# Optimization experiments

Measured on AMD Instinct MI355X. Metric: run time of the kernel, lower is better.

The kernel has to match this reference:

```python
import jax, jax.numpy as jnp
import numpy as np

B, N, H = 2, 2048, 1024
NUM_HEADS = 16
HEAD_DIM = H // NUM_HEADS
SCALE = HEAD_DIM ** -0.5


def setup_inputs() -> dict:
    key = jax.random.key(0)
    k1, k2, k3, k4 = jax.random.split(key, 4)
    s = 0.02
    return {
        "x": jax.random.normal(k1, (B, N, H), dtype=jnp.float32),
        "x2": jax.random.normal(k2, (B, N, H), dtype=jnp.float32),
        "Wqkv": jax.random.normal(k3, (H, 3 * H), dtype=jnp.float32) * s,
        "Wout": jax.random.normal(k4, (H, H), dtype=jnp.float32) * s,
        "bout": jnp.zeros((H,), dtype=jnp.float32),
    }


def _split_qkv(t):
    # t: [B, N, 3H] -> [3, B, h, N, d]
    b, n, _ = t.shape
    t = t.reshape(b, n, 3, NUM_HEADS, HEAD_DIM)
    return jnp.transpose(t, (2, 0, 3, 1, 4))


def reference(x, x2, Wqkv, Wout, bout):
    # shared qkv projection applied to both streams (bias=False)
    qkv2 = _split_qkv(x2 @ Wqkv)  # k, v from x2
    k, v = qkv2[1], qkv2[2]       # [B, h, N2, d]
    qkv1 = _split_qkv(x @ Wqkv)   # q from x
    q = qkv1[0]                   # [B, h, N, d]

    att = jax.nn.softmax(jnp.einsum("bhxd,bhyd->bhxy", q, k) * SCALE, axis=-1)
    out = jnp.einsum("bhxy,bhyd->bhxd", att, v)        # [B, h, N, d]
    out = jnp.transpose(out, (0, 2, 1, 3)).reshape(x.shape[0], x.shape[1], -1)
    return out @ Wout + bout
```

## Files before the change

### kernel.cpp

```cpp
#include <hip/hip_runtime.h>

#define B_ 2
#define N_ 2048
#define H_ 1024
#define NH_ 16
#define D_ 64

typedef _Float16 f16;
typedef _Float16 f16x4 __attribute__((ext_vector_type(4)));
typedef _Float16 f16x8 __attribute__((ext_vector_type(8)));
typedef float f32x4 __attribute__((ext_vector_type(4)));

#define MFMA16(a, b, c) __builtin_amdgcn_mfma_f32_16x16x32_f16((a), (b), (c), 0, 0, 0)

__device__ __forceinline__ void cp16(void* lds, const void* g) {
  __builtin_amdgcn_global_load_lds(
      (const __attribute__((address_space(1))) void*)g,
      (__attribute__((address_space(3))) void*)lds, 16, 0, 0);
}

__global__ __launch_bounds__(256) void convf16(
    const float* __restrict__ a, const float* __restrict__ b,
    f16* __restrict__ ao, f16* __restrict__ bo) {
  const size_t i = ((size_t)blockIdx.x * 256 + threadIdx.x) * 8;
  const float* __restrict__ src = (blockIdx.y == 0) ? a : b;
  f16* __restrict__ dst = (blockIdx.y == 0) ? ao : bo;
  float4 v0 = ((const float4*)(src + i))[0];
  float4 v1 = ((const float4*)(src + i))[1];
  f16x8 o;
  o[0] = (f16)v0.x; o[1] = (f16)v0.y; o[2] = (f16)v0.z; o[3] = (f16)v0.w;
  o[4] = (f16)v1.x; o[5] = (f16)v1.y; o[6] = (f16)v1.z; o[7] = (f16)v1.w;
  *(f16x8*)(dst + i) = o;
}

__global__ __launch_bounds__(256) void transw(
    const float* __restrict__ W, f16* __restrict__ Wt, int rows, int ncols) {
  const int cb = blockIdx.x * 64, kb = blockIdx.y * 64;
  const int t = threadIdx.x;
  __shared__ f16 T[64][72];
  {
    const int k = t >> 2, c0 = (t & 3) * 16;
    const float* wp = W + (size_t)(kb + k) * ncols + cb + c0;
    float4 w0 = ((const float4*)wp)[0];
    float4 w1 = ((const float4*)wp)[1];
    float4 w2 = ((const float4*)wp)[2];
    float4 w3 = ((const float4*)wp)[3];
    T[c0 + 0][k] = (f16)w0.x;  T[c0 + 1][k] = (f16)w0.y;
    T[c0 + 2][k] = (f16)w0.z;  T[c0 + 3][k] = (f16)w0.w;
    T[c0 + 4][k] = (f16)w1.x;  T[c0 + 5][k] = (f16)w1.y;
    T[c0 + 6][k] = (f16)w1.z;  T[c0 + 7][k] = (f16)w1.w;
    T[c0 + 8][k] = (f16)w2.x;  T[c0 + 9][k] = (f16)w2.y;
    T[c0 + 10][k] = (f16)w2.z; T[c0 + 11][k] = (f16)w2.w;
    T[c0 + 12][k] = (f16)w3.x; T[c0 + 13][k] = (f16)w3.y;
    T[c0 + 14][k] = (f16)w3.z; T[c0 + 15][k] = (f16)w3.w;
  }
  __syncthreads();
  {
    const int c = t >> 2, k0 = (t & 3) * 16;
    f16* op = Wt + (size_t)(cb + c) * rows + kb + k0;
    *(f16x8*)(op + 0) = *(const f16x8*)(&T[c][k0]);
    *(f16x8*)(op + 8) = *(const f16x8*)(&T[c][k0 + 8]);
  }
}

__global__ __launch_bounds__(256) void transv(
    const f16* __restrict__ V, f16* __restrict__ Vt) {
  const int nb = blockIdx.x * 64, bh = blockIdx.y;
  const int t = threadIdx.x;
  __shared__ f16 T[64][72];
  {
    const int n = t >> 2, d0 = (t & 3) * 16;
    const f16* vp = V + ((size_t)bh * N_ + nb + n) * D_ + d0;
    f16x8 v0 = *(const f16x8*)(vp);
    f16x8 v1 = *(const f16x8*)(vp + 8);
#pragma unroll
    for (int i = 0; i < 8; ++i) T[d0 + i][n] = v0[i];
#pragma unroll
    for (int i = 0; i < 8; ++i) T[d0 + 8 + i][n] = v1[i];
  }
  __syncthreads();
  {
    const int d = t >> 2, n0 = (t & 3) * 16;
    f16* op = Vt + ((size_t)bh * D_ + d) * N_ + nb + n0;
    *(f16x8*)(op + 0) = *(const f16x8*)(&T[d][n0]);
    *(f16x8*)(op + 8) = *(const f16x8*)(&T[d][n0 + 8]);
  }
}

__global__ __launch_bounds__(256) void qkv_mfma(
    const f16* __restrict__ Xc, const f16* __restrict__ X2c,
    const f16* __restrict__ Wt, f16* __restrict__ Qo,
    f16* __restrict__ Ko, f16* __restrict__ Vo) {
  const int bid = blockIdx.x;
  const int rb = (bid & 31) * 128;
  const int cb = (bid >> 5) * 128;
  const int t = threadIdx.x;
  const int lane = t & 63, wid = t >> 6;
  const int quad = lane >> 4, n16 = lane & 15;
  const int wm = wid >> 1, wn = wid & 1;

  const f16* __restrict__ A = (cb < H_) ? Xc : X2c;
  const int seg = cb >> 10;
  const float qscale = (seg == 0) ? 0.125f * 1.44269504f : 1.0f;
  f16* __restrict__ outp = (seg == 0) ? Qo : (seg == 1 ? Ko : Vo);

  __shared__ f16 As[128 * 32];
  __shared__ f16 Bs[128 * 32];

  f32x4 acc[4][4];
#pragma unroll
  for (int i = 0; i < 4; ++i)
#pragma unroll
    for (int j = 0; j < 4; ++j) acc[i][j] = (f32x4){0.f, 0.f, 0.f, 0.f};

  int srow0 = wid * 16 + (lane >> 2);
  int srow1 = 64 + srow0;
  int gl0 = ((lane & 3) ^ ((srow0 >> 1) & 3)) * 8;
  int gl1 = ((lane & 3) ^ ((srow1 >> 1) & 3)) * 8;
  const f16* gA0 = A + (size_t)(rb + srow0) * H_ + gl0;
  const f16* gA1 = A + (size_t)(rb + srow1) * H_ + gl1;
  const f16* gB0 = Wt + (size_t)(cb + srow0) * H_ + gl0;
  const f16* gB1 = Wt + (size_t)(cb + srow1) * H_ + gl1;
  f16* lA0 = &As[wid * 512];
  f16* lA1 = &As[2048 + wid * 512];
  f16* lB0 = &Bs[wid * 512];
  f16* lB1 = &Bs[2048 + wid * 512];

  const int fsw = (quad ^ ((n16 >> 1) & 3)) * 8;
  int aoff[4], boff[4];
#pragma unroll
  for (int i = 0; i < 4; ++i) {
    aoff[i] = (wm * 64 + i * 16 + n16) * 32 + fsw;
    boff[i] = (wn * 64 + i * 16 + n16) * 32 + fsw;
  }

  for (int kt = 0; kt < H_; kt += 32) {
    __syncthreads();
    cp16(lA0, gA0); cp16(lA1, gA1);
    cp16(lB0, gB0); cp16(lB1, gB1);
    gA0 += 32; gA1 += 32; gB0 += 32; gB1 += 32;
    __syncthreads();

    f16x8 af[4], bf[4];
#pragma unroll
    for (int mt = 0; mt < 4; ++mt) af[mt] = *(const f16x8*)(&As[aoff[mt]]);
#pragma unroll
    for (int nt = 0; nt < 4; ++nt) bf[nt] = *(const f16x8*)(&Bs[boff[nt]]);
#pragma unroll
    for (int mt = 0; mt < 4; ++mt)
#pragma unroll
      for (int nt = 0; nt < 4; ++nt)
        acc[mt][nt] = MFMA16(af[mt], bf[nt], acc[mt][nt]);
  }

#pragma unroll
  for (int mt = 0; mt < 4; ++mt)
#pragma unroll
    for (int nt = 0; nt < 4; ++nt)
#pragma unroll
      for (int r = 0; r < 4; ++r) {
        int grow = rb + wm * 64 + mt * 16 + quad * 4 + r;
        int gcol = cb + wn * 64 + nt * 16 + n16;
        int bb = grow >> 11, nn = grow & 2047;
        int hh = (gcol >> 6) & 15, dd = gcol & 63;
        outp[(((size_t)(bb * NH_ + hh)) * N_ + nn) * D_ + dd] =
            (f16)(acc[mt][nt][r] * qscale);
      }
}

__global__ __launch_bounds__(256) void attn2(
    const f16* __restrict__ Q, const f16* __restrict__ K,
    const f16* __restrict__ Vt, f16* __restrict__ AO) {
  const int bh = blockIdx.y;
  const int b = bh >> 4, h = bh & 15;
  const int qb = blockIdx.x * 128;
  const int t = threadIdx.x;
  const int lane = t & 63, wid = t >> 6;
  const int quad = lane >> 4, n16 = lane & 15;

  const f16* __restrict__ Qp = Q + (size_t)bh * N_ * D_;
  const f16* __restrict__ Kp = K + (size_t)bh * N_ * D_;
  const f16* __restrict__ Vp = Vt + (size_t)bh * D_ * N_;

  __shared__ f16 Ks[64 * 64];
  __shared__ f16 Vs[64 * 64];
  __shared__ f16 Ps[4][32 * 72];

  f16x8 qf[2][2];
#pragma unroll
  for (int qc = 0; qc < 2; ++qc) {
    const f16* qp = Qp + (size_t)(qb + wid * 32 + qc * 16 + n16) * D_ + quad * 8;
    qf[qc][0] = *(const f16x8*)(qp);
    qf[qc][1] = *(const f16x8*)(qp + 32);
  }

  f32x4 o[2][4];
#pragma unroll
  for (int i = 0; i < 2; ++i)
#pragma unroll
    for (int j = 0; j < 4; ++j) o[i][j] = (f32x4){0.f, 0.f, 0.f, 0.f};
  float lsum[2] = {0.f, 0.f};

  int srow0 = wid * 8 + (lane >> 3);
  int srow1 = 32 + srow0;
  int gl0 = ((lane & 7) ^ (srow0 & 7)) * 8;
  int gl1 = ((lane & 7) ^ (srow1 & 7)) * 8;
  const f16* gK0 = Kp + (size_t)srow0 * D_ + gl0;
  const f16* gK1 = Kp + (size_t)srow1 * D_ + gl1;
  const f16* gV0 = Vp + (size_t)srow0 * N_ + gl0;
  const f16* gV1 = Vp + (size_t)srow1 * N_ + gl1;
  f16* lK0 = &Ks[wid * 512];
  f16* lK1 = &Ks[2048 + wid * 512];
  f16* lV0 = &Vs[wid * 512];
  f16* lV1 = &Vs[2048 + wid * 512];

  const int fs0 = (quad ^ (n16 & 7)) * 8;
  const int fs1 = ((quad + 4) ^ (n16 & 7)) * 8;

  for (int kt = 0; kt < N_; kt += 64) {
    __syncthreads();
    cp16(lK0, gK0); cp16(lK1, gK1);
    cp16(lV0, gV0); cp16(lV1, gV1);
    gK0 += 64 * D_; gK1 += 64 * D_; gV0 += 64; gV1 += 64;
    __syncthreads();

    f32x4 s[4][2];
#pragma unroll
    for (int kc = 0; kc < 4; ++kc) {
      const f16x8 kf0 = *(const f16x8*)(&Ks[(kc * 16 + n16) * 64 + fs0]);
      const f16x8 kf1 = *(const f16x8*)(&Ks[(kc * 16 + n16) * 64 + fs1]);
#pragma unroll
      for (int qc = 0; qc < 2; ++qc) {
        f32x4 sv = (f32x4){0.f, 0.f, 0.f, 0.f};
        sv = MFMA16(kf0, qf[qc][0], sv);
        sv = MFMA16(kf1, qf[qc][1], sv);
        s[kc][qc] = sv;
      }
    }

    f16* __restrict__ pw = Ps[wid];
#pragma unroll
    for (int qc = 0; qc < 2; ++qc) {
      float ls = 0.f;
#pragma unroll
      for (int kc = 0; kc < 4; ++kc) {
        f16x4 pk;
#pragma unroll
        for (int r = 0; r < 4; ++r) {
          float p = __builtin_amdgcn_exp2f(s[kc][qc][r]);
          ls += p;
          pk[r] = (f16)p;
        }
        *(f16x4*)(&pw[(qc * 16 + n16) * 72 + kc * 16 + quad * 4]) = pk;
      }
      lsum[qc] += ls;
    }

    f16x8 vf[4][2];
#pragma unroll
    for (int dt = 0; dt < 4; ++dt) {
      vf[dt][0] = *(const f16x8*)(&Vs[(dt * 16 + n16) * 64 + fs0]);
      vf[dt][1] = *(const f16x8*)(&Vs[(dt * 16 + n16) * 64 + fs1]);
    }
#pragma unroll
    for (int mq = 0; mq < 2; ++mq) {
      const f16x8 pa0 = *(const f16x8*)(&pw[(mq * 16 + n16) * 72 + quad * 8]);
      const f16x8 pa1 = *(const f16x8*)(&pw[(mq * 16 + n16) * 72 + 32 + quad * 8]);
#pragma unroll
      for (int dt = 0; dt < 4; ++dt) {
        o[mq][dt] = MFMA16(pa0, vf[dt][0], o[mq][dt]);
        o[mq][dt] = MFMA16(pa1, vf[dt][1], o[mq][dt]);
      }
    }
  }

#pragma unroll
  for (int qc = 0; qc < 2; ++qc) {
    lsum[qc] += __shfl_xor(lsum[qc], 16);
    lsum[qc] += __shfl_xor(lsum[qc], 32);
  }

#pragma unroll
  for (int mq = 0; mq < 2; ++mq)
#pragma unroll
    for (int r = 0; r < 4; ++r) {
      float inv = 1.0f / __shfl(lsum[mq], quad * 4 + r);
      int nrow = qb + wid * 32 + mq * 16 + quad * 4 + r;
      f16* aop = AO + ((size_t)(b * N_ + nrow)) * H_ + h * 64;
#pragma unroll
      for (int dt = 0; dt < 4; ++dt)
        aop[dt * 16 + n16] = (f16)(o[mq][dt][r] * inv);
    }
}

__global__ __launch_bounds__(256) void out_mfma(
    const f16* __restrict__ A, const f16* __restrict__ Wt,
    const float* __restrict__ bias, float* __restrict__ out) {
  const int bid = blockIdx.x;
  const int rb = (bid & 31) * 128;
  const int cb = (bid >> 5) * 128;
  const int t = threadIdx.x;
  const int lane = t & 63, wid = t >> 6;
  const int quad = lane >> 4, n16 = lane & 15;
  const int wm = wid >> 1, wn = wid & 1;

  __shared__ f16 As[128 * 32];
  __shared__ f16 Bs[128 * 32];

  f32x4 acc[4][4];
#pragma unroll
  for (int i = 0; i < 4; ++i)
#pragma unroll
    for (int j = 0; j < 4; ++j) acc[i][j] = (f32x4){0.f, 0.f, 0.f, 0.f};

  int srow0 = wid * 16 + (lane >> 2);
  int srow1 = 64 + srow0;
  int gl0 = ((lane & 3) ^ ((srow0 >> 1) & 3)) * 8;
  int gl1 = ((lane & 3) ^ ((srow1 >> 1) & 3)) * 8;
  const f16* gA0 = A + (size_t)(rb + srow0) * H_ + gl0;
  const f16* gA1 = A + (size_t)(rb + srow1) * H_ + gl1;
  const f16* gB0 = Wt + (size_t)(cb + srow0) * H_ + gl0;
  const f16* gB1 = Wt + (size_t)(cb + srow1) * H_ + gl1;
  f16* lA0 = &As[wid * 512];
  f16* lA1 = &As[2048 + wid * 512];
  f16* lB0 = &Bs[wid * 512];
  f16* lB1 = &Bs[2048 + wid * 512];

  const int fsw = (quad ^ ((n16 >> 1) & 3)) * 8;
  int aoff[4], boff[4];
#pragma unroll
  for (int i = 0; i < 4; ++i) {
    aoff[i] = (wm * 64 + i * 16 + n16) * 32 + fsw;
    boff[i] = (wn * 64 + i * 16 + n16) * 32 + fsw;
  }

  for (int kt = 0; kt < H_; kt += 32) {
    __syncthreads();
    cp16(lA0, gA0); cp16(lA1, gA1);
    cp16(lB0, gB0); cp16(lB1, gB1);
    gA0 += 32; gA1 += 32; gB0 += 32; gB1 += 32;
    __syncthreads();

    f16x8 af[4], bf[4];
#pragma unroll
    for (int mt = 0; mt < 4; ++mt) af[mt] = *(const f16x8*)(&As[aoff[mt]]);
#pragma unroll
    for (int nt = 0; nt < 4; ++nt) bf[nt] = *(const f16x8*)(&Bs[boff[nt]]);
#pragma unroll
    for (int mt = 0; mt < 4; ++mt)
#pragma unroll
      for (int nt = 0; nt < 4; ++nt)
        acc[mt][nt] = MFMA16(af[mt], bf[nt], acc[mt][nt]);
  }

#pragma unroll
  for (int nt = 0; nt < 4; ++nt) {
    int gcol = cb + wn * 64 + nt * 16 + n16;
    float bv = bias[gcol];
#pragma unroll
    for (int mt = 0; mt < 4; ++mt)
#pragma unroll
      for (int r = 0; r < 4; ++r) {
        int grow = rb + wm * 64 + mt * 16 + quad * 4 + r;
        out[(size_t)grow * H_ + gcol] = acc[mt][nt][r] + bv;
      }
  }
}

extern "C" void kernel_launch(void* const* d_in, const int* in_sizes, int n_in,
                              void* d_out, int out_size, void* d_ws, size_t ws_size,
                              hipStream_t stream) {
  const float* x    = (const float*)d_in[0];
  const float* x2   = (const float*)d_in[1];
  const float* Wqkv = (const float*)d_in[2];
  const float* Wout = (const float*)d_in[3];
  const float* bout = (const float*)d_in[4];
  float* out = (float*)d_out;

  const size_t per = (size_t)B_ * NH_ * N_ * D_;
  f16* Xc    = (f16*)d_ws;
  f16* X2c   = Xc + per;
  f16* Qw    = X2c + per;
  f16* Kw    = Qw + per;
  f16* Vw    = Kw + per;
  f16* Vtw   = Vw + per;
  f16* AO    = Vtw + per;
  f16* WqkvT = AO + per;
  f16* WoutT = WqkvT + (size_t)3072 * 1024;

  convf16<<<dim3(2048, 2), 256, 0, stream>>>(x, x2, Xc, X2c);
  transw<<<dim3(48, 16), 256, 0, stream>>>(Wqkv, WqkvT, H_, 3 * H_);
  transw<<<dim3(16, 16), 256, 0, stream>>>(Wout, WoutT, H_, H_);
  qkv_mfma<<<dim3(768), 256, 0, stream>>>(Xc, X2c, WqkvT, Qw, Kw, Vw);
  transv<<<dim3(32, 32), 256, 0, stream>>>(Vw, Vtw);
  attn2<<<dim3(16, 32), 256, 0, stream>>>(Qw, Kw, Vtw, AO);
  out_mfma<<<dim3(256), 256, 0, stream>>>(AO, WoutT, bout, out);
}
```

Before: 205.3 us.

## Split attention KV range across wave pairs and keep P in registers

The attention kernel now gives each block 64 query rows instead of 128 and splits every 128-key step between two wave pairs. Each pair handles one 64-key half, and the two partial outputs and row sums are combined through LDS at the end. The softmax probabilities stay in registers and feed a 16x16x16 MFMA directly, with V fragments read from LDS, so the per-wave P staging buffer and its round trip are gone. This doubles the grid to 1024 blocks for better occupancy, at the cost of twice the Q-side K/V reloading, a final cross-wave reduction, and the smaller-K MFMA instruction.

```diff
diff --git a/kernel.cpp b/kernel.cpp
--- a/kernel.cpp
+++ b/kernel.cpp
@@ -12,6 +12,7 @@
 typedef float f32x4 __attribute__((ext_vector_type(4)));
 
 #define MFMA16(a, b, c) __builtin_amdgcn_mfma_f32_16x16x32_f16((a), (b), (c), 0, 0, 0)
+#define MFMA16K(a, b, c) __builtin_amdgcn_mfma_f32_16x16x16f16((a), (b), (c), 0, 0, 0)
 
 __device__ __forceinline__ void cp16(void* lds, const void* g) {
   __builtin_amdgcn_global_load_lds(
@@ -168,28 +169,29 @@
       }
 }
 
-__global__ __launch_bounds__(256) void attn2(
+__global__ __launch_bounds__(256) void attn4(
     const f16* __restrict__ Q, const f16* __restrict__ K,
     const f16* __restrict__ Vt, f16* __restrict__ AO) {
   const int bh = blockIdx.y;
   const int b = bh >> 4, h = bh & 15;
-  const int qb = blockIdx.x * 128;
+  const int qb = blockIdx.x * 64;
   const int t = threadIdx.x;
   const int lane = t & 63, wid = t >> 6;
   const int quad = lane >> 4, n16 = lane & 15;
+  const int qh = wid & 1;
+  const int kh = wid >> 1;
 
   const f16* __restrict__ Qp = Q + (size_t)bh * N_ * D_;
   const f16* __restrict__ Kp = K + (size_t)bh * N_ * D_;
   const f16* __restrict__ Vp = Vt + (size_t)bh * D_ * N_;
 
-  __shared__ f16 Ks[64 * 64];
-  __shared__ f16 Vs[64 * 64];
-  __shared__ f16 Ps[4][32 * 72];
+  __shared__ f16 Ks[2][64 * 64];
+  __shared__ f16 Vs[2][64 * 64];
 
   f16x8 qf[2][2];
 #pragma unroll
   for (int qc = 0; qc < 2; ++qc) {
-    const f16* qp = Qp + (size_t)(qb + wid * 32 + qc * 16 + n16) * D_ + quad * 8;
+    const f16* qp = Qp + (size_t)(qb + qh * 32 + qc * 16 + n16) * D_ + quad * 8;
     qf[qc][0] = *(const f16x8*)(qp);
     qf[qc][1] = *(const f16x8*)(qp + 32);
   }
@@ -201,96 +203,117 @@
     for (int j = 0; j < 4; ++j) o[i][j] = (f32x4){0.f, 0.f, 0.f, 0.f};
   float lsum[2] = {0.f, 0.f};
 
-  int srow0 = wid * 8 + (lane >> 3);
-  int srow1 = 32 + srow0;
-  int gl0 = ((lane & 7) ^ (srow0 & 7)) * 8;
-  int gl1 = ((lane & 7) ^ (srow1 & 7)) * 8;
+  const int srow0 = wid * 8 + (lane >> 3);
+  const int srow1 = 32 + srow0;
+  const int gl0 = ((lane & 7) ^ (srow0 & 7)) * 8;
+  const int gl1 = ((lane & 7) ^ (srow1 & 7)) * 8;
   const f16* gK0 = Kp + (size_t)srow0 * D_ + gl0;
   const f16* gK1 = Kp + (size_t)srow1 * D_ + gl1;
   const f16* gV0 = Vp + (size_t)srow0 * N_ + gl0;
   const f16* gV1 = Vp + (size_t)srow1 * N_ + gl1;
-  f16* lK0 = &Ks[wid * 512];
-  f16* lK1 = &Ks[2048 + wid * 512];
-  f16* lV0 = &Vs[wid * 512];
-  f16* lV1 = &Vs[2048 + wid * 512];
 
   const int fs0 = (quad ^ (n16 & 7)) * 8;
   const int fs1 = ((quad + 4) ^ (n16 & 7)) * 8;
-
-  for (int kt = 0; kt < N_; kt += 64) {
-    __syncthreads();
-    cp16(lK0, gK0); cp16(lK1, gK1);
-    cp16(lV0, gV0); cp16(lV1, gV1);
-    gK0 += 64 * D_; gK1 += 64 * D_; gV0 += 64; gV1 += 64;
-    __syncthreads();
-
-    f32x4 s[4][2];
+  int voff[4];
+#pragma unroll
+  for (int kc = 0; kc < 4; ++kc)
+    voff[kc] = n16 * 64 + (((kc * 2 + (quad >> 1)) ^ (n16 & 7)) * 8) + (quad & 1) * 4;
+
+  const f16* __restrict__ ks = &Ks[kh][0];
+  const f16* __restrict__ vs = &Vs[kh][0];
+
+  for (int kt = 0; kt < N_; kt += 128) {
+    __syncthreads();
+    cp16(&Ks[0][wid * 512], gK0 + (size_t)kt * D_);
+    cp16(&Ks[0][2048 + wid * 512], gK1 + (size_t)kt * D_);
+    cp16(&Ks[1][wid * 512], gK0 + (size_t)(kt + 64) * D_);
+    cp16(&Ks[1][2048 + wid * 512], gK1 + (size_t)(kt + 64) * D_);
+    cp16(&Vs[0][wid * 512], gV0 + kt);
+    cp16(&Vs[0][2048 + wid * 512], gV1 + kt);
+    cp16(&Vs[1][wid * 512], gV0 + kt + 64);
+    cp16(&Vs[1][2048 + wid * 512], gV1 + kt + 64);
+    __syncthreads();
+
+    f32x4 s[2][4];
 #pragma unroll
     for (int kc = 0; kc < 4; ++kc) {
-      const f16x8 kf0 = *(const f16x8*)(&Ks[(kc * 16 + n16) * 64 + fs0]);
-      const f16x8 kf1 = *(const f16x8*)(&Ks[(kc * 16 + n16) * 64 + fs1]);
+      const f16x8 kf0 = *(const f16x8*)(&ks[(kc * 16 + n16) * 64 + fs0]);
+      const f16x8 kf1 = *(const f16x8*)(&ks[(kc * 16 + n16) * 64 + fs1]);
 #pragma unroll
       for (int qc = 0; qc < 2; ++qc) {
         f32x4 sv = (f32x4){0.f, 0.f, 0.f, 0.f};
         sv = MFMA16(kf0, qf[qc][0], sv);
         sv = MFMA16(kf1, qf[qc][1], sv);
-        s[kc][qc] = sv;
+        s[qc][kc] = sv;
       }
     }
 
-    f16* __restrict__ pw = Ps[wid];
+    f16x4 pa[2][4];
+#pragma unroll
+    for (int qc = 0; qc < 2; ++qc)
+#pragma unroll
+      for (int kc = 0; kc < 4; ++kc)
+#pragma unroll
+        for (int r = 0; r < 4; ++r) {
+          float p = __builtin_amdgcn_exp2f(s[qc][kc][r]);
+          lsum[qc] += p;
+          pa[qc][kc][r] = (f16)p;
+        }
+
+#pragma unroll
+    for (int kc = 0; kc < 4; ++kc)
+#pragma unroll
+      for (int dt = 0; dt < 4; ++dt) {
+        const f16x4 vb = *(const f16x4*)(&vs[dt * 1024 + voff[kc]]);
+        o[0][dt] = MFMA16K(pa[0][kc], vb, o[0][dt]);
+        o[1][dt] = MFMA16K(pa[1][kc], vb, o[1][dt]);
+      }
+  }
+
+  __syncthreads();
+  float* red = (float*)&Ks[0][0];
+  if (kh == 1) {
+    float* p = red + ((size_t)qh * 64 + lane) * 36;
+#pragma unroll
+    for (int qc = 0; qc < 2; ++qc)
+#pragma unroll
+      for (int dt = 0; dt < 4; ++dt)
+        *(f32x4*)(p + (qc * 4 + dt) * 4) = o[qc][dt];
+    p[32] = lsum[0];
+    p[33] = lsum[1];
+  }
+  __syncthreads();
+  if (kh == 0) {
+    const float* p = red + ((size_t)qh * 64 + lane) * 36;
+#pragma unroll
+    for (int qc = 0; qc < 2; ++qc)
+#pragma unroll
+      for (int dt = 0; dt < 4; ++dt) {
+        f32x4 v = *(const f32x4*)(p + (qc * 4 + dt) * 4);
+#pragma unroll
+        for (int r = 0; r < 4; ++r) o[qc][dt][r] += v[r];
+      }
+    lsum[0] += p[32];
+    lsum[1] += p[33];
+
 #pragma unroll
     for (int qc = 0; qc < 2; ++qc) {
-      float ls = 0.f;
-#pragma unroll
-      for (int kc = 0; kc < 4; ++kc) {
-        f16x4 pk;
-#pragma unroll
-        for (int r = 0; r < 4; ++r) {
-          float p = __builtin_amdgcn_exp2f(s[kc][qc][r]);
-          ls += p;
-          pk[r] = (f16)p;
-        }
-        *(f16x4*)(&pw[(qc * 16 + n16) * 72 + kc * 16 + quad * 4]) = pk;
-      }
-      lsum[qc] += ls;
+      lsum[qc] += __shfl_xor(lsum[qc], 16);
+      lsum[qc] += __shfl_xor(lsum[qc], 32);
     }
 
-    f16x8 vf[4][2];
-#pragma unroll
-    for (int dt = 0; dt < 4; ++dt) {
-      vf[dt][0] = *(const f16x8*)(&Vs[(dt * 16 + n16) * 64 + fs0]);
-      vf[dt][1] = *(const f16x8*)(&Vs[(dt * 16 + n16) * 64 + fs1]);
-    }
-#pragma unroll
-    for (int mq = 0; mq < 2; ++mq) {
-      const f16x8 pa0 = *(const f16x8*)(&pw[(mq * 16 + n16) * 72 + quad * 8]);
-      const f16x8 pa1 = *(const f16x8*)(&pw[(mq * 16 + n16) * 72 + 32 + quad * 8]);
-#pragma unroll
-      for (int dt = 0; dt < 4; ++dt) {
-        o[mq][dt] = MFMA16(pa0, vf[dt][0], o[mq][dt]);
-        o[mq][dt] = MFMA16(pa1, vf[dt][1], o[mq][dt]);
-      }
-    }
-  }
-
-#pragma unroll
-  for (int qc = 0; qc < 2; ++qc) {
-    lsum[qc] += __shfl_xor(lsum[qc], 16);
-    lsum[qc] += __shfl_xor(lsum[qc], 32);
-  }
-
-#pragma unroll
-  for (int mq = 0; mq < 2; ++mq)
-#pragma unroll
-    for (int r = 0; r < 4; ++r) {
-      float inv = 1.0f / __shfl(lsum[mq], quad * 4 + r);
-      int nrow = qb + wid * 32 + mq * 16 + quad * 4 + r;
-      f16* aop = AO + ((size_t)(b * N_ + nrow)) * H_ + h * 64;
-#pragma unroll
-      for (int dt = 0; dt < 4; ++dt)
-        aop[dt * 16 + n16] = (f16)(o[mq][dt][r] * inv);
-    }
+#pragma unroll
+    for (int qc = 0; qc < 2; ++qc)
+#pragma unroll
+      for (int r = 0; r < 4; ++r) {
+        float inv = 1.0f / __shfl(lsum[qc], quad * 4 + r);
+        int nrow = qb + qh * 32 + qc * 16 + quad * 4 + r;
+        f16* aop = AO + ((size_t)(b * N_ + nrow)) * H_ + h * 64;
+#pragma unroll
+        for (int dt = 0; dt < 4; ++dt)
+          aop[dt * 16 + n16] = (f16)(o[qc][dt][r] * inv);
+      }
+  }
 }
 
 __global__ __launch_bounds__(256) void out_mfma(
@@ -393,6 +416,6 @@
   transw<<<dim3(16, 16), 256, 0, stream>>>(Wout, WoutT, H_, H_);
   qkv_mfma<<<dim3(768), 256, 0, stream>>>(Xc, X2c, WqkvT, Qw, Kw, Vw);
   transv<<<dim3(32, 32), 256, 0, stream>>>(Vw, Vtw);
-  attn2<<<dim3(16, 32), 256, 0, stream>>>(Qw, Kw, Vtw, AO);
+  attn4<<<dim3(32, 32), 256, 0, stream>>>(Qw, Kw, Vtw, AO);
   out_mfma<<<dim3(256), 256, 0, stream>>>(AO, WoutT, bout, out);
 }
```

After: 217.9 us. 1.06x slower.
